# Kernel optimization log

Hardware: AMD Instinct MI355X
Metric: run time of the kernel (lower is better)

## Reference

```python
import jax, jax.numpy as jnp
import numpy as np

E = 23  # unique experts
K = 3   # activated experts per token


def setup_inputs() -> dict:
    key = jax.random.key(0)
    ks = jax.random.split(key, 8)
    B, S, D, H = 4, 1024, 1024, 768
    sd = 1.0 / np.sqrt(D)
    sh = 1.0 / np.sqrt(H)
    return {
        "x": jax.random.normal(ks[0], (B, S, D), jnp.float32),
        "gate_W": jax.random.normal(ks[1], (D, E), jnp.float32) * sd,
        "gate_b": jnp.zeros((E,), jnp.float32),
        "route_bias": jnp.zeros((E,), jnp.float32),  # registered buffer 'bias'
        "W1": jax.random.normal(ks[2], (E, D, H), jnp.float32) * sd,
        "b1": jnp.zeros((E, H), jnp.float32),
        "W2": jax.random.normal(ks[3], (E, H, D), jnp.float32) * sh,
        "b2": jnp.zeros((E, D), jnp.float32),
        "sW1": jax.random.normal(ks[4], (D, H), jnp.float32) * sd,
        "sb1": jnp.zeros((H,), jnp.float32),
        "sW2": jax.random.normal(ks[5], (H, D), jnp.float32) * sh,
        "sb2": jnp.zeros((D,), jnp.float32),
    }


def _gelu(x):
    return jax.nn.gelu(x, approximate=False)  # torch nn.GELU default = exact erf


def reference(x, gate_W, gate_b, route_bias, W1, b1, W2, b2, sW1, sb1, sW2, sb2):
    o_shape = x.shape
    xt = x.reshape(-1, o_shape[-1])                       # [N, D]
    N = xt.shape[0]
    gate_weights = jax.nn.sigmoid(xt @ gate_W + gate_b)   # [N, E]
    _, top_idx = jax.lax.top_k(gate_weights + route_bias, K)  # [N, K]
    top_w = jnp.take_along_axis(gate_weights, top_idx, axis=-1)
    top_w = top_w / top_w.sum(axis=-1, keepdims=True)     # [N, K]
    onehot = jax.nn.one_hot(top_idx, E, dtype=xt.dtype)   # [N, K, E]
    combine = jnp.einsum('nke,nk->ne', onehot, top_w)     # [N, E] routed weights
    counts = onehot.sum(axis=(0, 1))                      # tokens per expert
    # dense-equivalent grouped expert MLPs (same math as gather/split/concat)
    h = _gelu(jnp.einsum('nd,edh->enh', xt, W1) + b1[:, None, :])   # [E, N, H]
    y = jnp.einsum('enh,ehd->end', h, W2) + b2[:, None, :]          # [E, N, D]
    routed = jnp.einsum('end,ne->nd', y, combine)
    shared = _gelu(xt @ sW1 + sb1) @ sW2 + sb2
    out = shared + routed
    # aux load-balance loss
    gw_norm = gate_weights / gate_weights.sum(axis=-1, keepdims=True)
    P = gw_norm.mean(axis=0)
    Fvec = (E * counts) / (K * N)
    aux_loss = (P * Fvec).sum()
    return out.reshape(o_shape), aux_loss
```

## Files before the change

kernel.cpp:

```cpp
#include <hip/hip_runtime.h>
#include <hip/hip_bf16.h>
#include <stdint.h>

#define N_TOK 4096
#define DDIM  1024
#define HDIM  768
#define NEXP  23
#define TOPK  3
#define MAXTILE 152
#define SLOTS   19456

typedef float floatx4 __attribute__((ext_vector_type(4)));
typedef short short8  __attribute__((ext_vector_type(8)));

__device__ __forceinline__ short f2bf(float f) {
    __hip_bfloat16 h = __float2bfloat16(f);
    return *reinterpret_cast<short*>(&h);
}
__device__ __forceinline__ float bf2f(short s) {
    unsigned u = ((unsigned)(unsigned short)s) << 16;
    return __uint_as_float(u);
}
__device__ __forceinline__ float gelu_erf(float v) {
    return 0.5f * v * (1.0f + erff(v * 0.70710678118654752f));
}
__device__ __forceinline__ void gl_lds16(const short* g, short* l) {
    __builtin_amdgcn_global_load_lds(
        (const __attribute__((address_space(1))) void*)g,
        (__attribute__((address_space(3))) void*)l, 16, 0, 0);
}

__global__ __launch_bounds__(256) void gate_kernel(
    const float* __restrict__ x, const float* __restrict__ gate_W,
    const float* __restrict__ gate_b, const float* __restrict__ route_bias,
    int* __restrict__ top_idx, float* __restrict__ top_w,
    float* __restrict__ psum_part)
{
    const int wave = threadIdx.x >> 6, lane = threadIdx.x & 63;
    const int n = blockIdx.x * 4 + wave;

    __shared__ float gw[64][25];
    float acc[NEXP];
#pragma unroll
    for (int e = 0; e < NEXP; e++) acc[e] = 0.f;

    const float* xr = x + (size_t)n * DDIM;
    for (int c0 = 0; c0 < DDIM; c0 += 64) {
        for (int idx = threadIdx.x; idx < 64 * NEXP; idx += 256)
            gw[idx / NEXP][idx % NEXP] = gate_W[(size_t)c0 * NEXP + idx];
        __syncthreads();
        float xd = xr[c0 + lane];
#pragma unroll
        for (int e = 0; e < NEXP; e++) acc[e] += xd * gw[lane][e];
        __syncthreads();
    }
    for (int off = 32; off > 0; off >>= 1) {
#pragma unroll
        for (int e = 0; e < NEXP; e++) acc[e] += __shfl_xor(acc[e], off, 64);
    }

    float p[NEXP], s = 0.f;
#pragma unroll
    for (int e = 0; e < NEXP; e++) {
        p[e] = 1.f / (1.f + expf(-(acc[e] + gate_b[e])));
        s += p[e];
    }
    const float inv = 1.f / s;

    __shared__ float ps[4][NEXP];
    if (lane == 0) {
#pragma unroll
        for (int e = 0; e < NEXP; e++) ps[wave][e] = p[e] * inv;
        int idx[TOPK]; float w[TOPK]; bool used[NEXP] = {};
        for (int k = 0; k < TOPK; k++) {
            float best = -1e30f; int bi = 0;
            for (int e = 0; e < NEXP; e++) {
                if (!used[e]) {
                    float sc = p[e] + route_bias[e];
                    if (sc > best) { best = sc; bi = e; }
                }
            }
            used[bi] = true; idx[k] = bi; w[k] = p[bi];
        }
        float wsum = w[0] + w[1] + w[2];
        for (int k = 0; k < TOPK; k++) {
            top_idx[n * TOPK + k] = idx[k];
            top_w[n * TOPK + k]   = w[k] / wsum;
        }
    }
    __syncthreads();
    if (threadIdx.x < NEXP) {
        int e = threadIdx.x;
        psum_part[(size_t)blockIdx.x * NEXP + e] =
            ps[0][e] + ps[1][e] + ps[2][e] + ps[3][e];
    }
}

__global__ __launch_bounds__(256) void plan_kernel(
    const int* __restrict__ top_idx, const float* __restrict__ psum_part,
    int* __restrict__ poff, int* __restrict__ cursor, int* __restrict__ tile_e,
    int* __restrict__ Ptot, float* __restrict__ out_aux)
{
    __shared__ int   cnt[NEXP];
    __shared__ float psum[NEXP];
    const int t = threadIdx.x;
    if (t < NEXP) { cnt[t] = 0; psum[t] = 0.f; }
    __syncthreads();

    for (int i = t; i < N_TOK * TOPK; i += 256)
        atomicAdd(&cnt[top_idx[i]], 1);

    float loc[NEXP];
#pragma unroll
    for (int e = 0; e < NEXP; e++) loc[e] = 0.f;
    for (int b = t; b < N_TOK / 4; b += 256) {
        const float* row = psum_part + (size_t)b * NEXP;
#pragma unroll
        for (int e = 0; e < NEXP; e++) loc[e] += row[e];
    }
#pragma unroll
    for (int e = 0; e < NEXP; e++) atomicAdd(&psum[e], loc[e]);
    __syncthreads();

    if (t == 0) {
        int off = 0, nt = 0; float aux = 0.f;
        for (int e = 0; e < NEXP; e++) {
            poff[e] = off; cursor[e] = 0;
            float P = psum[e] / (float)N_TOK;
            float F = (float)NEXP * (float)cnt[e] / ((float)TOPK * (float)N_TOK);
            aux += P * F;
            int tiles = (cnt[e] + 127) >> 7;
            for (int i = 0; i < tiles; i++) tile_e[nt++] = e;
            off += tiles << 7;
        }
        poff[NEXP] = off;
        *Ptot = off;
        for (int i = 0; i < N_TOK / 128; i++) tile_e[nt++] = NEXP;
        while (nt < MAXTILE) tile_e[nt++] = -1;
        *out_aux = aux;
    }
}

__global__ __launch_bounds__(256) void scatter_kernel(
    const int* __restrict__ top_idx, const int* __restrict__ poff,
    int* __restrict__ cursor, int* __restrict__ tok_of_slot,
    int* __restrict__ slot_of_tok, const int* __restrict__ Ptot)
{
    int n = blockIdx.x * 256 + threadIdx.x;
    for (int k = 0; k < TOPK; k++) {
        int e = top_idx[n * TOPK + k];
        int pos = atomicAdd(&cursor[e], 1);
        int slot = poff[e] + pos;
        tok_of_slot[slot] = n;
        slot_of_tok[n * 4 + k] = slot;
    }
    int P = *Ptot;
    tok_of_slot[P + n] = n;
    slot_of_tok[n * 4 + 3] = P + n;
}

__global__ __launch_bounds__(256) void prep_kernel(
    const float* __restrict__ x, short* __restrict__ xb,
    const float* __restrict__ b1, const float* __restrict__ sb1,
    const float* __restrict__ b2, const float* __restrict__ sb2,
    float* __restrict__ bias1_all, float* __restrict__ bias2_all)
{
    const int b = blockIdx.x;
    if (b < N_TOK) {
        size_t i = (size_t)b * 256 + threadIdx.x;
        float4 v = ((const float4*)x)[i];
        short4 o;
        o.x = f2bf(v.x); o.y = f2bf(v.y); o.z = f2bf(v.z); o.w = f2bf(v.w);
        ((short4*)xb)[i] = o;
    } else if (b == N_TOK) {
        short4 z; z.x = 0; z.y = 0; z.z = 0; z.w = 0;
        ((short4*)(xb + (size_t)N_TOK * DDIM))[threadIdx.x] = z;
    } else {
        int i = (b - N_TOK - 1) * 256 + threadIdx.x;
        if (i < 24 * HDIM) {
            bias1_all[i] = (i < NEXP * HDIM) ? b1[i] : sb1[i - NEXP * HDIM];
        } else {
            int j = i - 24 * HDIM;
            if (j < 24 * DDIM)
                bias2_all[j] = (j < NEXP * DDIM) ? b2[j] : sb2[j - NEXP * DDIM];
        }
    }
}

__global__ __launch_bounds__(256) void tcvt_kernel(
    const float* __restrict__ src, const float* __restrict__ ssrc,
    short* __restrict__ dst, int R, int C)
{
    __shared__ short tile[64][72];
    const int e = blockIdx.z;
    const float* s = (e < NEXP) ? src + (size_t)e * R * C : ssrc;
    short* d = dst + (size_t)e * R * C;
    const int c0 = blockIdx.x * 64, r0 = blockIdx.y * 64;
    const int t = threadIdx.x;

    const int rr = t >> 4, cc = (t & 15) << 2;
#pragma unroll
    for (int i = 0; i < 64; i += 16) {
        float4 v = *(const float4*)&s[(size_t)(r0 + i + rr) * C + c0 + cc];
        tile[cc + 0][i + rr] = f2bf(v.x);
        tile[cc + 1][i + rr] = f2bf(v.y);
        tile[cc + 2][i + rr] = f2bf(v.z);
        tile[cc + 3][i + rr] = f2bf(v.w);
    }
    __syncthreads();
    const int cc2 = t >> 3, rr2 = (t & 7) << 3;
#pragma unroll
    for (int j = 0; j < 64; j += 32) {
        *(short8*)&d[(size_t)(c0 + j + cc2) * R + r0 + rr2] =
            *(const short8*)&tile[j + cc2][rr2];
    }
}

template <bool FFN1>
__global__ __launch_bounds__(256) void gemm_kernel(
    const short* __restrict__ Abase, const int* __restrict__ tok_of_slot,
    const int* __restrict__ tile_e, const short* __restrict__ Wall,
    const float* __restrict__ bias_all, const short* __restrict__ zrow,
    short* __restrict__ outb)
{
    constexpr int KD = FFN1 ? DDIM : HDIM;
    constexpr int NC = FFN1 ? HDIM : DDIM;

    const int tile = blockIdx.y;
    const int e = tile_e[tile];
    if (e < 0) return;
    const int slot0 = tile * 128;
    const int n0 = blockIdx.x * 128;

    __shared__ short As[128 * 32];
    __shared__ short Bs[128 * 32];

    const int t = threadIdx.x;
    const int w = t >> 6, l = t & 63;
    const int quad = l >> 4, l16 = l & 15;
    const int wr = w >> 1, wc = w & 1;

    const int ra0 = w * 32 + (l >> 2);
    const int ra1 = ra0 + 16;
    const int ko  = (l & 3) << 3;

    const short *ap0, *ap1;
    if constexpr (FFN1) {
        int t0 = tok_of_slot[slot0 + ra0];
        int t1 = tok_of_slot[slot0 + ra1];
        ap0 = (t0 >= 0) ? Abase + (size_t)t0 * KD : zrow;
        ap1 = (t1 >= 0) ? Abase + (size_t)t1 * KD : zrow;
    } else {
        ap0 = Abase + (size_t)(slot0 + ra0) * KD;
        ap1 = Abase + (size_t)(slot0 + ra1) * KD;
    }
    ap0 += ko; ap1 += ko;
    const short* bbase = Wall + (size_t)e * NC * KD + (size_t)n0 * KD;
    const short* bp0 = bbase + (size_t)ra0 * KD + ko;
    const short* bp1 = bbase + (size_t)ra1 * KD + ko;

    short* asd0 = As + (w * 32) * 32;
    short* asd1 = As + (w * 32 + 16) * 32;
    short* bsd0 = Bs + (w * 32) * 32;
    short* bsd1 = Bs + (w * 32 + 16) * 32;

    floatx4 acc[4][4] = {};

    for (int k0 = 0; k0 < KD; k0 += 32) {
        gl_lds16(ap0, asd0); gl_lds16(ap1, asd1);
        gl_lds16(bp0, bsd0); gl_lds16(bp1, bsd1);
        ap0 += 32; ap1 += 32; bp0 += 32; bp1 += 32;
        __syncthreads();

        short8 af[4], bf[4];
#pragma unroll
        for (int i = 0; i < 4; i++)
            af[i] = *(const short8*)&As[(wr * 64 + i * 16 + l16) * 32 + quad * 8];
#pragma unroll
        for (int j = 0; j < 4; j++)
            bf[j] = *(const short8*)&Bs[(wc * 64 + j * 16 + l16) * 32 + quad * 8];
#pragma unroll
        for (int i = 0; i < 4; i++)
#pragma unroll
            for (int j = 0; j < 4; j++)
                acc[i][j] = __builtin_amdgcn_mfma_f32_16x16x32_bf16(af[i], bf[j], acc[i][j], 0, 0, 0);
        __syncthreads();
    }

    const int bias_off = e * NC;
#pragma unroll
    for (int j = 0; j < 4; j++) {
        const int col = n0 + wc * 64 + j * 16 + l16;
        const float bv = bias_all[bias_off + col];
#pragma unroll
        for (int i = 0; i < 4; i++)
#pragma unroll
            for (int r = 0; r < 4; r++) {
                const int row = slot0 + wr * 64 + i * 16 + quad * 4 + r;
                float v = acc[i][j][r] + bv;
                outb[(size_t)row * NC + col] = f2bf(FFN1 ? gelu_erf(v) : v);
            }
    }
}

__global__ __launch_bounds__(256) void combine_kernel(
    const short* __restrict__ ybuf, const int* __restrict__ slot_of_tok,
    const float* __restrict__ top_w, float* __restrict__ out)
{
    const int n = blockIdx.x;
    const int c = threadIdx.x;
    const int s0 = slot_of_tok[n * 4 + 0];
    const int s1 = slot_of_tok[n * 4 + 1];
    const int s2 = slot_of_tok[n * 4 + 2];
    const int ss = slot_of_tok[n * 4 + 3];
    const float w0 = top_w[n * 3 + 0];
    const float w1 = top_w[n * 3 + 1];
    const float w2 = top_w[n * 3 + 2];

    short4 y0 = ((const short4*)(ybuf + (size_t)s0 * DDIM))[c];
    short4 y1 = ((const short4*)(ybuf + (size_t)s1 * DDIM))[c];
    short4 y2 = ((const short4*)(ybuf + (size_t)s2 * DDIM))[c];
    short4 ys = ((const short4*)(ybuf + (size_t)ss * DDIM))[c];

    float4 o;
    o.x = bf2f(ys.x) + w0 * bf2f(y0.x) + w1 * bf2f(y1.x) + w2 * bf2f(y2.x);
    o.y = bf2f(ys.y) + w0 * bf2f(y0.y) + w1 * bf2f(y1.y) + w2 * bf2f(y2.y);
    o.z = bf2f(ys.z) + w0 * bf2f(y0.z) + w1 * bf2f(y1.z) + w2 * bf2f(y2.z);
    o.w = bf2f(ys.w) + w0 * bf2f(y0.w) + w1 * bf2f(y1.w) + w2 * bf2f(y2.w);
    ((float4*)(out + (size_t)n * DDIM))[c] = o;
}

extern "C" void kernel_launch(void* const* d_in, const int* in_sizes, int n_in,
                              void* d_out, int out_size, void* d_ws, size_t ws_size,
                              hipStream_t stream)
{
    const float* x          = (const float*)d_in[0];
    const float* gate_W     = (const float*)d_in[1];
    const float* gate_b     = (const float*)d_in[2];
    const float* route_bias = (const float*)d_in[3];
    const float* W1         = (const float*)d_in[4];
    const float* b1         = (const float*)d_in[5];
    const float* W2         = (const float*)d_in[6];
    const float* b2         = (const float*)d_in[7];
    const float* sW1        = (const float*)d_in[8];
    const float* sb1        = (const float*)d_in[9];
    const float* sW2        = (const float*)d_in[10];
    const float* sb2        = (const float*)d_in[11];
    float* out = (float*)d_out;

    uint8_t* ws = (uint8_t*)d_ws;
    int*   top_idx   = (int*)(ws);
    float* top_w     = (float*)(ws + 49152);
    int*   poff      = (int*)(ws + 98304);
    int*   cursor    = (int*)(ws + 98432);
    int*   Ptot      = (int*)(ws + 98560);
    int*   tile_e    = (int*)(ws + 98688);
    float* psum_part = (float*)(ws + 99328);
    int*   tok_slot  = (int*)(ws + 193536);
    int*   slot_tok  = (int*)(ws + 271360);
    float* bias1_all = (float*)(ws + 336896);
    float* bias2_all = (float*)(ws + 410624);
    short* xb        = (short*)(ws + 512000);
    short* W1T       = (short*)(ws + 8902656);
    short* W2T       = (short*)(ws + 46651392);
    short* hbuf      = (short*)(ws + 84400128);
    short* ybuf      = (short*)(ws + 512000);
    const short* zrow = xb + (size_t)N_TOK * DDIM;

    hipMemsetAsync(tok_slot, 0xFF, SLOTS * sizeof(int), stream);

    prep_kernel<<<N_TOK + 1 + (24 * (HDIM + DDIM) + 255) / 256, 256, 0, stream>>>(
        x, xb, b1, sb1, b2, sb2, bias1_all, bias2_all);
    tcvt_kernel<<<dim3(HDIM / 64, DDIM / 64, 24), 256, 0, stream>>>(
        W1, sW1, W1T, DDIM, HDIM);
    tcvt_kernel<<<dim3(DDIM / 64, HDIM / 64, 24), 256, 0, stream>>>(
        W2, sW2, W2T, HDIM, DDIM);

    gate_kernel<<<N_TOK / 4, 256, 0, stream>>>(x, gate_W, gate_b, route_bias,
                                               top_idx, top_w, psum_part);
    plan_kernel<<<1, 256, 0, stream>>>(top_idx, psum_part, poff, cursor, tile_e,
                                       Ptot, out + (size_t)N_TOK * DDIM);
    scatter_kernel<<<N_TOK / 256, 256, 0, stream>>>(top_idx, poff, cursor,
                                                    tok_slot, slot_tok, Ptot);

    gemm_kernel<true><<<dim3(HDIM / 128, MAXTILE), 256, 0, stream>>>(
        xb, tok_slot, tile_e, W1T, bias1_all, zrow, hbuf);
    gemm_kernel<false><<<dim3(DDIM / 128, MAXTILE), 256, 0, stream>>>(
        hbuf, tok_slot, tile_e, W2T, bias2_all, zrow, ybuf);
    combine_kernel<<<N_TOK, 256, 0, stream>>>(ybuf, slot_tok, top_w, out);
}
```

Measured before the change: 492.6 us.

## Triple-buffer GEMM LDS loads and fuse prep/gate and weight-convert launches

The grouped GEMM now uses a three-stage LDS ring filled by global_load_lds. Explicit vmcnt waits and barriers let loads for later K-steps overlap the MFMA work on the current step, instead of syncing twice per step on one buffer. The x-to-bf16 and bias-prep work is folded into the gate kernel launch, and the two weight transpose-convert launches become one. The tok_slot memset and the zero row are removed: out-of-range token indices are clamped to token 0, and the tile-to-expert map is now filled in parallel. This trades more LDS per block and hand-written waitcnt logic for fewer launches and better latency hiding. Padding rows read arbitrary token data, but only those rows' outputs are affected.

```diff
diff --git a/kernel.cpp b/kernel.cpp
--- a/kernel.cpp
+++ b/kernel.cpp
@@ -30,14 +30,38 @@
         (__attribute__((address_space(3))) void*)l, 16, 0, 0);
 }
 
-__global__ __launch_bounds__(256) void gate_kernel(
+__global__ __launch_bounds__(256) void prep_gate_kernel(
     const float* __restrict__ x, const float* __restrict__ gate_W,
     const float* __restrict__ gate_b, const float* __restrict__ route_bias,
     int* __restrict__ top_idx, float* __restrict__ top_w,
-    float* __restrict__ psum_part)
-{
+    float* __restrict__ psum_part, short* __restrict__ xb,
+    const float* __restrict__ b1, const float* __restrict__ sb1,
+    const float* __restrict__ b2, const float* __restrict__ sb2,
+    float* __restrict__ bias1_all, float* __restrict__ bias2_all)
+{
+    const int b = blockIdx.x;
+    if (b >= 1024) {
+        const int bb = b - 1024;
+        if (bb < N_TOK) {
+            size_t i = (size_t)bb * 256 + threadIdx.x;
+            float4 v = ((const float4*)x)[i];
+            short4 o;
+            o.x = f2bf(v.x); o.y = f2bf(v.y); o.z = f2bf(v.z); o.w = f2bf(v.w);
+            ((short4*)xb)[i] = o;
+        } else {
+            int i = (bb - N_TOK) * 256 + threadIdx.x;
+            if (i < 24 * HDIM) {
+                bias1_all[i] = (i < NEXP * HDIM) ? b1[i] : sb1[i - NEXP * HDIM];
+            } else {
+                int j = i - 24 * HDIM;
+                if (j < 24 * DDIM)
+                    bias2_all[j] = (j < NEXP * DDIM) ? b2[j] : sb2[j - NEXP * DDIM];
+            }
+        }
+        return;
+    }
     const int wave = threadIdx.x >> 6, lane = threadIdx.x & 63;
-    const int n = blockIdx.x * 4 + wave;
+    const int n = b * 4 + wave;
 
     __shared__ float gw[64][25];
     float acc[NEXP];
@@ -91,7 +115,7 @@
     __syncthreads();
     if (threadIdx.x < NEXP) {
         int e = threadIdx.x;
-        psum_part[(size_t)blockIdx.x * NEXP + e] =
+        psum_part[(size_t)b * NEXP + e] =
             ps[0][e] + ps[1][e] + ps[2][e] + ps[3][e];
     }
 }
@@ -103,6 +127,7 @@
 {
     __shared__ int   cnt[NEXP];
     __shared__ float psum[NEXP];
+    __shared__ int   tbase[NEXP + 1];
     const int t = threadIdx.x;
     if (t < NEXP) { cnt[t] = 0; psum[t] = 0.f; }
     __syncthreads();
@@ -123,21 +148,28 @@
     __syncthreads();
 
     if (t == 0) {
-        int off = 0, nt = 0; float aux = 0.f;
+        int tb = 0; float aux = 0.f;
         for (int e = 0; e < NEXP; e++) {
-            poff[e] = off; cursor[e] = 0;
+            tbase[e] = tb;
             float P = psum[e] / (float)N_TOK;
             float F = (float)NEXP * (float)cnt[e] / ((float)TOPK * (float)N_TOK);
             aux += P * F;
-            int tiles = (cnt[e] + 127) >> 7;
-            for (int i = 0; i < tiles; i++) tile_e[nt++] = e;
-            off += tiles << 7;
+            tb += (cnt[e] + 127) >> 7;
         }
-        poff[NEXP] = off;
-        *Ptot = off;
-        for (int i = 0; i < N_TOK / 128; i++) tile_e[nt++] = NEXP;
-        while (nt < MAXTILE) tile_e[nt++] = -1;
+        tbase[NEXP] = tb;
+        *Ptot = tb << 7;
         *out_aux = aux;
+    }
+    __syncthreads();
+    const int tr = tbase[NEXP];
+    if (t < NEXP) { poff[t] = tbase[t] << 7; cursor[t] = 0; }
+    for (int i = t; i < MAXTILE; i += 256) {
+        int v = -1;
+        if (i < tr) {
+            for (int e = 0; e < NEXP; e++)
+                if (i >= tbase[e] && i < tbase[e + 1]) v = e;
+        } else if (i < tr + N_TOK / 128) v = NEXP;
+        tile_e[i] = v;
     }
 }
 
@@ -159,43 +191,25 @@
     slot_of_tok[n * 4 + 3] = P + n;
 }
 
-__global__ __launch_bounds__(256) void prep_kernel(
-    const float* __restrict__ x, short* __restrict__ xb,
-    const float* __restrict__ b1, const float* __restrict__ sb1,
-    const float* __restrict__ b2, const float* __restrict__ sb2,
-    float* __restrict__ bias1_all, float* __restrict__ bias2_all)
-{
-    const int b = blockIdx.x;
-    if (b < N_TOK) {
-        size_t i = (size_t)b * 256 + threadIdx.x;
-        float4 v = ((const float4*)x)[i];
-        short4 o;
-        o.x = f2bf(v.x); o.y = f2bf(v.y); o.z = f2bf(v.z); o.w = f2bf(v.w);
-        ((short4*)xb)[i] = o;
-    } else if (b == N_TOK) {
-        short4 z; z.x = 0; z.y = 0; z.z = 0; z.w = 0;
-        ((short4*)(xb + (size_t)N_TOK * DDIM))[threadIdx.x] = z;
+__global__ __launch_bounds__(256) void tcvt_kernel(
+    const float* __restrict__ W1, const float* __restrict__ sW1, short* __restrict__ W1T,
+    const float* __restrict__ W2, const float* __restrict__ sW2, short* __restrict__ W2T)
+{
+    __shared__ short tile[64][72];
+    const int z = blockIdx.z;
+    int R, C; const float* s; short* d;
+    if (z < 24) {
+        R = DDIM; C = HDIM;
+        s = (z < NEXP) ? W1 + (size_t)z * DDIM * HDIM : sW1;
+        d = W1T + (size_t)z * DDIM * HDIM;
     } else {
-        int i = (b - N_TOK - 1) * 256 + threadIdx.x;
-        if (i < 24 * HDIM) {
-            bias1_all[i] = (i < NEXP * HDIM) ? b1[i] : sb1[i - NEXP * HDIM];
-        } else {
-            int j = i - 24 * HDIM;
-            if (j < 24 * DDIM)
-                bias2_all[j] = (j < NEXP * DDIM) ? b2[j] : sb2[j - NEXP * DDIM];
-        }
-    }
-}
-
-__global__ __launch_bounds__(256) void tcvt_kernel(
-    const float* __restrict__ src, const float* __restrict__ ssrc,
-    short* __restrict__ dst, int R, int C)
-{
-    __shared__ short tile[64][72];
-    const int e = blockIdx.z;
-    const float* s = (e < NEXP) ? src + (size_t)e * R * C : ssrc;
-    short* d = dst + (size_t)e * R * C;
+        const int e = z - 24;
+        R = HDIM; C = DDIM;
+        s = (e < NEXP) ? W2 + (size_t)e * HDIM * DDIM : sW2;
+        d = W2T + (size_t)e * HDIM * DDIM;
+    }
     const int c0 = blockIdx.x * 64, r0 = blockIdx.y * 64;
+    if (c0 >= C || r0 >= R) return;
     const int t = threadIdx.x;
 
     const int rr = t >> 4, cc = (t & 15) << 2;
@@ -220,11 +234,11 @@
 __global__ __launch_bounds__(256) void gemm_kernel(
     const short* __restrict__ Abase, const int* __restrict__ tok_of_slot,
     const int* __restrict__ tile_e, const short* __restrict__ Wall,
-    const float* __restrict__ bias_all, const short* __restrict__ zrow,
-    short* __restrict__ outb)
+    const float* __restrict__ bias_all, short* __restrict__ outb)
 {
     constexpr int KD = FFN1 ? DDIM : HDIM;
     constexpr int NC = FFN1 ? HDIM : DDIM;
+    constexpr int KI = KD / 32;
 
     const int tile = blockIdx.y;
     const int e = tile_e[tile];
@@ -232,8 +246,8 @@
     const int slot0 = tile * 128;
     const int n0 = blockIdx.x * 128;
 
-    __shared__ short As[128 * 32];
-    __shared__ short Bs[128 * 32];
+    __shared__ short As[3][128 * 32];
+    __shared__ short Bs[3][128 * 32];
 
     const int t = threadIdx.x;
     const int w = t >> 6, l = t & 63;
@@ -248,43 +262,58 @@
     if constexpr (FFN1) {
         int t0 = tok_of_slot[slot0 + ra0];
         int t1 = tok_of_slot[slot0 + ra1];
-        ap0 = (t0 >= 0) ? Abase + (size_t)t0 * KD : zrow;
-        ap1 = (t1 >= 0) ? Abase + (size_t)t1 * KD : zrow;
+        t0 = ((unsigned)t0 < (unsigned)N_TOK) ? t0 : 0;
+        t1 = ((unsigned)t1 < (unsigned)N_TOK) ? t1 : 0;
+        ap0 = Abase + (size_t)t0 * KD + ko;
+        ap1 = Abase + (size_t)t1 * KD + ko;
     } else {
-        ap0 = Abase + (size_t)(slot0 + ra0) * KD;
-        ap1 = Abase + (size_t)(slot0 + ra1) * KD;
-    }
-    ap0 += ko; ap1 += ko;
+        ap0 = Abase + (size_t)(slot0 + ra0) * KD + ko;
+        ap1 = Abase + (size_t)(slot0 + ra1) * KD + ko;
+    }
     const short* bbase = Wall + (size_t)e * NC * KD + (size_t)n0 * KD;
     const short* bp0 = bbase + (size_t)ra0 * KD + ko;
     const short* bp1 = bbase + (size_t)ra1 * KD + ko;
 
-    short* asd0 = As + (w * 32) * 32;
-    short* asd1 = As + (w * 32 + 16) * 32;
-    short* bsd0 = Bs + (w * 32) * 32;
-    short* bsd1 = Bs + (w * 32 + 16) * 32;
+    const int ldo0 = (w * 32) * 32;
+    const int ldo1 = (w * 32 + 16) * 32;
 
     floatx4 acc[4][4] = {};
 
-    for (int k0 = 0; k0 < KD; k0 += 32) {
-        gl_lds16(ap0, asd0); gl_lds16(ap1, asd1);
-        gl_lds16(bp0, bsd0); gl_lds16(bp1, bsd1);
+#pragma unroll
+    for (int p = 0; p < 3; p++) {
+        gl_lds16(ap0, &As[p][ldo0]); gl_lds16(ap1, &As[p][ldo1]);
+        gl_lds16(bp0, &Bs[p][ldo0]); gl_lds16(bp1, &Bs[p][ldo1]);
         ap0 += 32; ap1 += 32; bp0 += 32; bp1 += 32;
-        __syncthreads();
-
+    }
+
+#pragma unroll
+    for (int k = 0; k < KI; k++) {
+        if (k < KI - 2)       asm volatile("s_waitcnt vmcnt(8)" ::: "memory");
+        else if (k == KI - 2) asm volatile("s_waitcnt vmcnt(4)" ::: "memory");
+        else                  asm volatile("s_waitcnt vmcnt(0)" ::: "memory");
+        asm volatile("s_barrier" ::: "memory");
+
+        const int s = k % 3;
         short8 af[4], bf[4];
 #pragma unroll
         for (int i = 0; i < 4; i++)
-            af[i] = *(const short8*)&As[(wr * 64 + i * 16 + l16) * 32 + quad * 8];
+            af[i] = *(const short8*)&As[s][(wr * 64 + i * 16 + l16) * 32 + quad * 8];
 #pragma unroll
         for (int j = 0; j < 4; j++)
-            bf[j] = *(const short8*)&Bs[(wc * 64 + j * 16 + l16) * 32 + quad * 8];
+            bf[j] = *(const short8*)&Bs[s][(wc * 64 + j * 16 + l16) * 32 + quad * 8];
 #pragma unroll
         for (int i = 0; i < 4; i++)
 #pragma unroll
             for (int j = 0; j < 4; j++)
                 acc[i][j] = __builtin_amdgcn_mfma_f32_16x16x32_bf16(af[i], bf[j], acc[i][j], 0, 0, 0);
-        __syncthreads();
+
+        asm volatile("s_waitcnt lgkmcnt(0)" ::: "memory");
+        asm volatile("s_barrier" ::: "memory");
+        if (k + 3 < KI) {
+            gl_lds16(ap0, &As[s][ldo0]); gl_lds16(ap1, &As[s][ldo1]);
+            gl_lds16(bp0, &Bs[s][ldo0]); gl_lds16(bp1, &Bs[s][ldo1]);
+            ap0 += 32; ap1 += 32; bp0 += 32; bp1 += 32;
+        }
     }
 
     const int bias_off = e * NC;
@@ -365,27 +394,19 @@
     short* W2T       = (short*)(ws + 46651392);
     short* hbuf      = (short*)(ws + 84400128);
     short* ybuf      = (short*)(ws + 512000);
-    const short* zrow = xb + (size_t)N_TOK * DDIM;
-
-    hipMemsetAsync(tok_slot, 0xFF, SLOTS * sizeof(int), stream);
-
-    prep_kernel<<<N_TOK + 1 + (24 * (HDIM + DDIM) + 255) / 256, 256, 0, stream>>>(
-        x, xb, b1, sb1, b2, sb2, bias1_all, bias2_all);
-    tcvt_kernel<<<dim3(HDIM / 64, DDIM / 64, 24), 256, 0, stream>>>(
-        W1, sW1, W1T, DDIM, HDIM);
-    tcvt_kernel<<<dim3(DDIM / 64, HDIM / 64, 24), 256, 0, stream>>>(
-        W2, sW2, W2T, HDIM, DDIM);
-
-    gate_kernel<<<N_TOK / 4, 256, 0, stream>>>(x, gate_W, gate_b, route_bias,
-                                               top_idx, top_w, psum_part);
+
+    prep_gate_kernel<<<1024 + N_TOK + (24 * (HDIM + DDIM)) / 256, 256, 0, stream>>>(
+        x, gate_W, gate_b, route_bias, top_idx, top_w, psum_part,
+        xb, b1, sb1, b2, sb2, bias1_all, bias2_all);
+    tcvt_kernel<<<dim3(16, 16, 48), 256, 0, stream>>>(W1, sW1, W1T, W2, sW2, W2T);
     plan_kernel<<<1, 256, 0, stream>>>(top_idx, psum_part, poff, cursor, tile_e,
                                        Ptot, out + (size_t)N_TOK * DDIM);
     scatter_kernel<<<N_TOK / 256, 256, 0, stream>>>(top_idx, poff, cursor,
                                                     tok_slot, slot_tok, Ptot);
 
     gemm_kernel<true><<<dim3(HDIM / 128, MAXTILE), 256, 0, stream>>>(
-        xb, tok_slot, tile_e, W1T, bias1_all, zrow, hbuf);
+        xb, tok_slot, tile_e, W1T, bias1_all, hbuf);
     gemm_kernel<false><<<dim3(DDIM / 128, MAXTILE), 256, 0, stream>>>(
-        hbuf, tok_slot, tile_e, W2T, bias2_all, zrow, ybuf);
+        hbuf, tok_slot, tile_e, W2T, bias2_all, ybuf);
     combine_kernel<<<N_TOK, 256, 0, stream>>>(ybuf, slot_tok, top_w, out);
 }
```

Result: no change. 483.5 us (-1.8%).
